# Kernel tuning notes

Hardware: AMD Instinct MI355X
Metric: run time of the kernel (lower is better)

Reference implementation:

```python
import math
import jax, jax.numpy as jnp
import numpy as np

D, NH, NL, NP = 256, 8, 3, 4
HD = D // NH
SHAPES = np.array([[92, 92], [46, 46], [23, 23]], dtype=np.int32)
LSI = np.concatenate([[0], np.cumsum(SHAPES[:, 0] * SHAPES[:, 1])[:-1]]).astype(np.int32)
LV = int((SHAPES[:, 0] * SHAPES[:, 1]).sum())  # 11109
B, LQ = 2, LV


def setup_inputs() -> dict:
    key = jax.random.key(0)
    ks = jax.random.split(key, 8)
    query = jax.random.normal(ks[0], (B, LQ, D), jnp.float32)
    reference_points = jax.random.uniform(ks[1], (B, LQ, NL, 2), dtype=jnp.float32)
    value_flat = jax.random.normal(ks[2], (B, LV, D), jnp.float32)
    # sampling_offsets: small random weight + structured directional bias (as in _reset_parameters)
    W_off = jax.random.normal(ks[3], (D, NH * NL * NP * 2), jnp.float32) * 0.01
    thetas = np.arange(NH, dtype=np.float64) * (2.0 * math.pi / NH)
    g = np.stack([np.cos(thetas), np.sin(thetas)], axis=-1)
    g = g / np.abs(g).max(axis=-1, keepdims=True)
    g = np.tile(g[:, None, None, :], (1, NL, NP, 1))
    g = g * (np.arange(NP) + 1)[None, None, :, None]
    b_off = jnp.asarray(g.reshape(-1), jnp.float32)
    W_attn = jax.random.normal(ks[4], (D, NH * NL * NP), jnp.float32) * 0.01
    b_attn = jnp.zeros((NH * NL * NP,), jnp.float32)
    W_val = jax.random.normal(ks[5], (D, D), jnp.float32) * (1.0 / math.sqrt(D))
    b_val = jnp.zeros((D,), jnp.float32)
    W_out = jax.random.normal(ks[6], (D, D), jnp.float32) * (1.0 / math.sqrt(D))
    b_out = jnp.zeros((D,), jnp.float32)
    return dict(query=query, reference_points=reference_points, value_flat=value_flat,
                W_val=W_val, b_val=b_val, W_off=W_off, b_off=b_off,
                W_attn=W_attn, b_attn=b_attn, W_out=W_out, b_out=b_out,
                spatial_shapes=jnp.asarray(SHAPES), level_start_index=jnp.asarray(LSI))


def _bilinear_sample(val_l, grid):
    """torch.F.grid_sample(mode='bilinear', padding_mode='zeros', align_corners=False).
    val_l: [B,H,W,nH,hd]; grid: [B,Q,nH,P,2] with (x,y) in [-1,1].
    Returns [B,nH,Q,P,hd]."""
    Bq, H, W, nH, hd = val_l.shape
    Q, P = grid.shape[1], grid.shape[3]
    x = ((grid[..., 0] + 1.0) * W - 1.0) * 0.5   # pixel coords, align_corners=False
    y = ((grid[..., 1] + 1.0) * H - 1.0) * 0.5
    x0f, y0f = jnp.floor(x), jnp.floor(y)
    lx, ly = x - x0f, y - y0f
    x0, y0 = x0f.astype(jnp.int32), y0f.astype(jnp.int32)
    val_bh = val_l.transpose(0, 3, 1, 2, 4).reshape(Bq * nH, H * W, hd)

    def corner(yi, xi, w):
        valid = (xi >= 0) & (xi < W) & (yi >= 0) & (yi < H)
        idx = jnp.clip(yi, 0, H - 1) * W + jnp.clip(xi, 0, W - 1)   # [B,Q,nH,P]
        idx_bh = idx.transpose(0, 2, 1, 3).reshape(Bq * nH, Q * P)
        g = jnp.take_along_axis(val_bh, idx_bh[:, :, None], axis=1)  # [B*nH, Q*P, hd]
        wm = (w * valid.astype(w.dtype)).transpose(0, 2, 1, 3).reshape(Bq * nH, Q * P, 1)
        return g * wm

    out = (corner(y0, x0, (1 - ly) * (1 - lx)) + corner(y0, x0 + 1, (1 - ly) * lx)
           + corner(y0 + 1, x0, ly * (1 - lx)) + corner(y0 + 1, x0 + 1, ly * lx))
    return out.reshape(Bq, nH, Q, P, hd)


def reference(query, reference_points, value_flat, W_val, b_val, W_off, b_off,
              W_attn, b_attn, W_out, b_out, spatial_shapes, level_start_index):
    shapes = np.asarray(spatial_shapes)          # static level geometry
    starts = np.asarray(level_start_index)
    Bq, Lq, _ = query.shape
    value = (value_flat @ W_val + b_val).reshape(Bq, -1, NH, HD)
    off = (query @ W_off + b_off).reshape(Bq, Lq, NH, NL, NP, 2)        # (dy,dx) pixels
    aw = jax.nn.softmax((query @ W_attn + b_attn).reshape(Bq, Lq, NH, NL * NP), axis=-1)
    aw = aw.reshape(Bq, Lq, NH, NL, NP)
    sh_f = jnp.asarray(shapes, jnp.float32)                              # [L,2] = (H,W)
    norm_off = off / sh_f[None, None, None, :, None, :]
    loc = reference_points[:, :, None, :, None, :] + norm_off           # [B,Lq,NH,NL,NP,2] (y,x)
    grid = 2.0 * loc[..., ::-1] - 1.0                                    # (x,y) in [-1,1]
    out = jnp.zeros((Bq, Lq, NH, HD), query.dtype)
    for l in range(NL):
        H, W = int(shapes[l, 0]), int(shapes[l, 1])
        s = int(starts[l])
        val_l = value[:, s:s + H * W].reshape(Bq, H, W, NH, HD)
        sampled = _bilinear_sample(val_l, grid[:, :, :, l])              # [B,NH,Lq,NP,HD]
        out = out + jnp.einsum('bhqpc,bqhp->bqhc', sampled, aw[:, :, :, l])
    return out.reshape(Bq, Lq, D) @ W_out + b_out
```

## Files before the change

kernel.cpp:

```cpp
#include <hip/hip_runtime.h>

#define LQn   11109
#define MTOT  22218

typedef __attribute__((ext_vector_type(8))) short short8;
typedef __attribute__((ext_vector_type(4))) float f32x4;

__device__ __forceinline__ unsigned short f2bf(float f) {
  union { float f; unsigned int u; } v; v.f = f;
  unsigned int r = v.u + 0x7fffu + ((v.u >> 16) & 1u);
  return (unsigned short)(r >> 16);
}

__device__ __forceinline__ int xcd_swz(int bid, int nwg) {
  const int xcd = bid & 7, pos = bid >> 3;
  const int q = nwg >> 3, r = nwg & 7;
  return (xcd < r ? xcd * (q + 1) : r * (q + 1) + (xcd - r) * q) + pos;
}

__global__ __launch_bounds__(256) void prep_weights(
    const float* __restrict__ Wval, const float* __restrict__ Woff,
    const float* __restrict__ Wattn, const float* __restrict__ Wout,
    const float* __restrict__ boff, const float* __restrict__ battn,
    unsigned short* __restrict__ Wval_t, unsigned short* __restrict__ Wcat_t,
    unsigned short* __restrict__ Wout_t, float* __restrict__ bcat) {
  int i = blockIdx.x * 256 + threadIdx.x;
  int n = i >> 8, k = i & 255;
  if (n < 256) {
    Wval_t[i] = f2bf(Wval[k * 256 + n]);
    Wout_t[i] = f2bf(Wout[k * 256 + n]);
  }
  float src = (n < 192) ? Woff[k * 192 + n] : Wattn[k * 96 + (n - 192)];
  Wcat_t[i] = f2bf(src);
  if (i < 288) bcat[i] = (i < 192) ? boff[i] : battn[i - 192];
}

__global__ __launch_bounds__(256) void gemm_fused12(
    const float* __restrict__ Aval,
    const float* __restrict__ Aq,
    const unsigned short* __restrict__ Bval,
    const unsigned short* __restrict__ Bcat,
    const float* __restrict__ bval, const float* __restrict__ bcat,
    unsigned short* __restrict__ value16,
    float* __restrict__ logits) {
  __shared__ unsigned short As[64][40];
  __shared__ unsigned short Bs[64][40];

  const int bm = blockIdx.x;
  int bn = blockIdx.y;
  const bool is2 = bn >= 4;
  if (is2) bn -= 4;
  const float* __restrict__ A = is2 ? Aq : Aval;
  const unsigned short* __restrict__ Bt = is2 ? Bcat : Bval;
  const float* __restrict__ bias = is2 ? bcat : bval;
  const int N = is2 ? 288 : 256;

  const int t = threadIdx.x;
  const int wave = t >> 6, lane = t & 63;
  const int wm = wave >> 1, wn = wave & 1;
  const int quad = lane >> 4, l16 = lane & 15;

  const int ldr = t >> 2;
  const int ldk = (t & 3) * 8;
  const int arow = bm * 64 + ldr;
  const int brow = bn * 64 + ldr;
  const bool aok = arow < MTOT;
  const bool bok = brow < N;
  const float* ap = A + (size_t)arow * 256 + ldk;
  const unsigned short* bp = Bt + (size_t)brow * 256 + ldk;

  f32x4 acc[2][2];
  for (int i = 0; i < 2; i++)
    for (int j = 0; j < 2; j++) acc[i][j] = (f32x4){0.f, 0.f, 0.f, 0.f};

  float4 a0c = {0.f,0.f,0.f,0.f}, a1c = a0c, a0n = a0c, a1n = a0c;
  uint4 bvc = {0u,0u,0u,0u}, bvn = bvc;
  if (aok) { a0c = *(const float4*)(ap);      a1c = *(const float4*)(ap + 4);
             a0n = *(const float4*)(ap + 32); a1n = *(const float4*)(ap + 36); }
  if (bok) { bvc = *(const uint4*)(bp);       bvn = *(const uint4*)(bp + 32); }

#pragma unroll
  for (int kb = 0; kb < 8; kb++) {
    ushort4 lo, hi;
    lo.x = f2bf(a0c.x); lo.y = f2bf(a0c.y); lo.z = f2bf(a0c.z); lo.w = f2bf(a0c.w);
    hi.x = f2bf(a1c.x); hi.y = f2bf(a1c.y); hi.z = f2bf(a1c.z); hi.w = f2bf(a1c.w);
    __syncthreads();
    *(ushort4*)(&As[ldr][ldk]) = lo;
    *(ushort4*)(&As[ldr][ldk + 4]) = hi;
    *(uint4*)(&Bs[ldr][ldk]) = bvc;
    __syncthreads();
    a0c = a0n; a1c = a1n; bvc = bvn;
    if (kb < 6) {
      const int k2 = (kb + 2) * 32;
      if (aok) { a0n = *(const float4*)(ap + k2); a1n = *(const float4*)(ap + k2 + 4); }
      if (bok) bvn = *(const uint4*)(bp + k2);
    }
    short8 af[2], bfr[2];
    for (int i = 0; i < 2; i++)
      af[i] = *(const short8*)(&As[wm * 32 + i * 16 + l16][quad * 8]);
    for (int j = 0; j < 2; j++)
      bfr[j] = *(const short8*)(&Bs[wn * 32 + j * 16 + l16][quad * 8]);
    for (int i = 0; i < 2; i++)
      for (int j = 0; j < 2; j++)
        acc[i][j] = __builtin_amdgcn_mfma_f32_16x16x32_bf16(af[i], bfr[j], acc[i][j], 0, 0, 0);
  }

  for (int i = 0; i < 2; i++)
    for (int j = 0; j < 2; j++) {
      int colg = bn * 64 + wn * 32 + j * 16 + l16;
      if (colg >= N) continue;
      float bsv = bias[colg];
      int row0 = bm * 64 + wm * 32 + i * 16 + quad * 4;
      for (int r = 0; r < 4; r++) {
        int rg = row0 + r;
        if (rg >= MTOT) continue;
        float v = acc[i][j][r] + bsv;
        if (is2) logits[(size_t)rg * 288 + colg] = v;
        else     value16[(size_t)rg * 256 + colg] = f2bf(v);
      }
    }
}

__global__ __launch_bounds__(256) void gemm_a16(
    const unsigned short* __restrict__ A,
    const unsigned short* __restrict__ Bt,
    const float* __restrict__ bias,
    float* __restrict__ C) {
  __shared__ unsigned short As[64][40];
  __shared__ unsigned short Bs[64][40];

  const int t = threadIdx.x;
  const int bm = blockIdx.x, bn = blockIdx.y;
  const int wave = t >> 6, lane = t & 63;
  const int wm = wave >> 1, wn = wave & 1;
  const int quad = lane >> 4, l16 = lane & 15;

  const int ldr = t >> 2;
  const int ldk = (t & 3) * 8;
  const int arow = bm * 64 + ldr;
  const int brow = bn * 64 + ldr;
  const bool aok = arow < MTOT;
  const unsigned short* ap = A + (size_t)arow * 256 + ldk;
  const unsigned short* bp = Bt + (size_t)brow * 256 + ldk;

  f32x4 acc[2][2];
  for (int i = 0; i < 2; i++)
    for (int j = 0; j < 2; j++) acc[i][j] = (f32x4){0.f, 0.f, 0.f, 0.f};

  uint4 avc = {0u,0u,0u,0u}, avn = avc, bvc, bvn;
  if (aok) { avc = *(const uint4*)(ap); avn = *(const uint4*)(ap + 32); }
  bvc = *(const uint4*)(bp);
  bvn = *(const uint4*)(bp + 32);

#pragma unroll
  for (int kb = 0; kb < 8; kb++) {
    __syncthreads();
    *(uint4*)(&As[ldr][ldk]) = avc;
    *(uint4*)(&Bs[ldr][ldk]) = bvc;
    __syncthreads();
    avc = avn; bvc = bvn;
    if (kb < 6) {
      const int k2 = (kb + 2) * 32;
      if (aok) avn = *(const uint4*)(ap + k2);
      bvn = *(const uint4*)(bp + k2);
    }
    short8 af[2], bfr[2];
    for (int i = 0; i < 2; i++)
      af[i] = *(const short8*)(&As[wm * 32 + i * 16 + l16][quad * 8]);
    for (int j = 0; j < 2; j++)
      bfr[j] = *(const short8*)(&Bs[wn * 32 + j * 16 + l16][quad * 8]);
    for (int i = 0; i < 2; i++)
      for (int j = 0; j < 2; j++)
        acc[i][j] = __builtin_amdgcn_mfma_f32_16x16x32_bf16(af[i], bfr[j], acc[i][j], 0, 0, 0);
  }

  for (int i = 0; i < 2; i++)
    for (int j = 0; j < 2; j++) {
      int colg = bn * 64 + wn * 32 + j * 16 + l16;
      float bsv = bias[colg];
      int row0 = bm * 64 + wm * 32 + i * 16 + quad * 4;
      for (int r = 0; r < 4; r++) {
        int rg = row0 + r;
        if (rg < MTOT)
          __builtin_nontemporal_store(acc[i][j][r] + bsv, &C[(size_t)rg * 256 + colg]);
      }
    }
}

__global__ __launch_bounds__(256) void msda_sample4(
    const unsigned short* __restrict__ value16,
    const float* __restrict__ logits,
    const float* __restrict__ refp,
    unsigned short* __restrict__ sampled) {
  __shared__ float          tw[8][96][4];
  __shared__ unsigned short ti[8][96][4];
  __shared__ float hmx[8][8], hrd[8][8];
  __shared__ float rfs[8][6];

  const int t = threadIdx.x;
  const int nbid = xcd_swz(blockIdx.x, gridDim.x);
  const int qbase = nbid * 8;

  if (t < 48) {
    int q = t / 6;
    if (qbase + q < MTOT) rfs[q][t - q * 6] = refp[(size_t)qbase * 6 + t];
  }
  if (t >= 64 && t < 128) {
    int tt = t - 64;
    int q = tt >> 3, h = tt & 7;
    int bq = qbase + q;
    if (bq < MTOT) {
      const float* lrow = logits + (size_t)bq * 288 + 192 + h * 12;
      float mx = -1e30f;
#pragma unroll
      for (int i = 0; i < 12; i++) mx = fmaxf(mx, __builtin_nontemporal_load(&lrow[i]));
      float den = 0.f;
#pragma unroll
      for (int i = 0; i < 12; i++)
        den += __expf(__builtin_nontemporal_load(&lrow[i]) - mx);
      hmx[q][h] = mx;
      hrd[q][h] = 1.0f / den;
    }
  }
  __syncthreads();

  {
    const int Hs[3] = {92, 46, 23};
    const int Ss[3] = {0, 8464, 10580};
#pragma unroll
    for (int r = 0; r < 3; r++) {
      const int task = t + r * 256;
      const int q = task / 96, s = task - q * 96;
      const int bq = qbase + q;
      if (bq < MTOT) {
        const int h = s / 12, pl = s - h * 12;
        const int l = pl >> 2;
        const int H = Hs[l], W = Hs[l], S = Ss[l];
        const float* lrow = logits + (size_t)bq * 288;
        const float aw = __expf(__builtin_nontemporal_load(&lrow[192 + s]) - hmx[q][h]) * hrd[q][h];
        const float offy = __builtin_nontemporal_load(&lrow[2 * s]);
        const float offx = __builtin_nontemporal_load(&lrow[2 * s + 1]);
        const float x = rfs[q][l * 2 + 1] * W + offx - 0.5f;
        const float y = rfs[q][l * 2 + 0] * H + offy - 0.5f;
        const float xf = floorf(x), yf = floorf(y);
        const int x0 = (int)xf, y0 = (int)yf;
        const float lx = x - xf, ly = y - yf;
        const bool xv0 = (x0 >= 0) & (x0 < W), xv1 = (x0 + 1 >= 0) & (x0 + 1 < W);
        const bool yv0 = (y0 >= 0) & (y0 < H), yv1 = (y0 + 1 >= 0) & (y0 + 1 < H);
        const int xc0 = min(max(x0, 0), W - 1), xc1 = min(max(x0 + 1, 0), W - 1);
        const int yc0 = min(max(y0, 0), H - 1), yc1 = min(max(y0 + 1, 0), H - 1);
        const int slot = pl * 8 + h;
        ti[q][slot][0] = (unsigned short)(S + yc0 * W + xc0);
        ti[q][slot][1] = (unsigned short)(S + yc0 * W + xc1);
        ti[q][slot][2] = (unsigned short)(S + yc1 * W + xc0);
        ti[q][slot][3] = (unsigned short)(S + yc1 * W + xc1);
        tw[q][slot][0] = (yv0 & xv0) ? aw * (1.f - ly) * (1.f - lx) : 0.f;
        tw[q][slot][1] = (yv0 & xv1) ? aw * (1.f - ly) * lx : 0.f;
        tw[q][slot][2] = (yv1 & xv0) ? aw * ly * (1.f - lx) : 0.f;
        tw[q][slot][3] = (yv1 & xv1) ? aw * ly * lx : 0.f;
      }
    }
  }
  __syncthreads();

  {
    const int w = t >> 6, lane = t & 63;
    const int q = w * 2 + (lane >> 5);
    const int h = (lane >> 2) & 7, cg = lane & 3;
    const int bq = qbase + q;
    const bool qv = bq < MTOT;
    const int bqc = qv ? bq : 0;
    const char* __restrict__ vb =
        (const char*)value16 + (size_t)(bqc / LQn) * ((size_t)LQn * 512);
    const unsigned laneoff = (unsigned)h * 64u + (unsigned)cg * 16u;

    float a0 = 0.f, a1 = 0.f, a2 = 0.f, a3 = 0.f;
    float a4 = 0.f, a5 = 0.f, a6 = 0.f, a7 = 0.f;
#pragma unroll
    for (int p = 0; p < 12; p++) {
      const int slot = p * 8 + h;
      const ushort4 tiv = *(const ushort4*)(&ti[q][slot][0]);
      const f32x4 wv = *(const f32x4*)(&tw[q][slot][0]);
#pragma unroll
      for (int k = 0; k < 4; k++) {
        const unsigned pix =
            (k == 0) ? tiv.x : (k == 1) ? tiv.y : (k == 2) ? tiv.z : tiv.w;
        const float wgt = wv[k];
        const uint4 u = *(const uint4*)(vb + ((pix << 9) + laneoff));
        a0 += wgt * __uint_as_float(u.x << 16);
        a1 += wgt * __uint_as_float(u.x & 0xffff0000u);
        a2 += wgt * __uint_as_float(u.y << 16);
        a3 += wgt * __uint_as_float(u.y & 0xffff0000u);
        a4 += wgt * __uint_as_float(u.z << 16);
        a5 += wgt * __uint_as_float(u.z & 0xffff0000u);
        a6 += wgt * __uint_as_float(u.w << 16);
        a7 += wgt * __uint_as_float(u.w & 0xffff0000u);
      }
    }
    if (qv) {
      uint4 o;
      o.x = (unsigned)f2bf(a0) | ((unsigned)f2bf(a1) << 16);
      o.y = (unsigned)f2bf(a2) | ((unsigned)f2bf(a3) << 16);
      o.z = (unsigned)f2bf(a4) | ((unsigned)f2bf(a5) << 16);
      o.w = (unsigned)f2bf(a6) | ((unsigned)f2bf(a7) << 16);
      *(uint4*)(sampled + (size_t)bq * 256 + h * 32 + cg * 8) = o;
    }
  }
}

extern "C" void kernel_launch(void* const* d_in, const int* in_sizes, int n_in,
                              void* d_out, int out_size, void* d_ws, size_t ws_size,
                              hipStream_t stream) {
  const float* query      = (const float*)d_in[0];
  const float* refp       = (const float*)d_in[1];
  const float* value_flat = (const float*)d_in[2];
  const float* W_val      = (const float*)d_in[3];
  const float* b_val      = (const float*)d_in[4];
  const float* W_off      = (const float*)d_in[5];
  const float* b_off      = (const float*)d_in[6];
  const float* W_attn     = (const float*)d_in[7];
  const float* b_attn     = (const float*)d_in[8];
  const float* W_out      = (const float*)d_in[9];
  const float* b_out      = (const float*)d_in[10];

  char* w = (char*)d_ws;
  size_t o = 0;
  auto carve = [&](size_t bytes) -> void* {
    void* p = (void*)(w + o);
    o += (bytes + 255) & ~(size_t)255;
    return p;
  };
  unsigned short* Wval_t  = (unsigned short*)carve(256 * 256 * 2);
  unsigned short* Wcat_t  = (unsigned short*)carve(288 * 256 * 2);
  unsigned short* Wout_t  = (unsigned short*)carve(256 * 256 * 2);
  float*          bcat    = (float*)carve(288 * 4);
  unsigned short* value16 = (unsigned short*)carve((size_t)MTOT * 256 * 2);
  float*          logits  = (float*)carve((size_t)MTOT * 288 * 4);
  unsigned short* samp_bf = (unsigned short*)carve((size_t)MTOT * 256 * 2);

  prep_weights<<<288, 256, 0, stream>>>(W_val, W_off, W_attn, W_out, b_off, b_attn,
                                        Wval_t, Wcat_t, Wout_t, bcat);

  const int mg = (MTOT + 63) / 64;
  dim3 g12(mg, 9);
  gemm_fused12<<<g12, 256, 0, stream>>>(value_flat, query, Wval_t, Wcat_t,
                                        b_val, bcat, value16, logits);

  const int sgrid = (MTOT + 7) / 8;
  msda_sample4<<<sgrid, 256, 0, stream>>>(value16, logits, refp, samp_bf);

  dim3 g3(mg, 4);
  gemm_a16<<<g3, 256, 0, stream>>>(samp_bf, Wout_t, b_out, (float*)d_out);
}
```

Before: 191.2 us.

## Fuse output projection GEMM into sampling kernel via shared-memory tile

The deformable-attention sampling kernel now writes its 8 query rows of bf16 samples into a shared-memory tile, reusing the weight/index scratch space. It then performs the output projection with MFMA directly from that tile, streaming W_out from global memory. This removes the intermediate sampled buffer round-trip and one kernel launch. The cost is that each block of 8 queries uses a 16-row MFMA with half the rows wasted and rereads the whole 256x256 W_out, relying on L2 hits. Nontemporal loads on logits are also replaced with ordinary loads.

```diff
diff --git a/kernel.cpp b/kernel.cpp
--- a/kernel.cpp
+++ b/kernel.cpp
@@ -121,79 +121,17 @@
     }
 }
 
-__global__ __launch_bounds__(256) void gemm_a16(
-    const unsigned short* __restrict__ A,
-    const unsigned short* __restrict__ Bt,
-    const float* __restrict__ bias,
-    float* __restrict__ C) {
-  __shared__ unsigned short As[64][40];
-  __shared__ unsigned short Bs[64][40];
-
-  const int t = threadIdx.x;
-  const int bm = blockIdx.x, bn = blockIdx.y;
-  const int wave = t >> 6, lane = t & 63;
-  const int wm = wave >> 1, wn = wave & 1;
-  const int quad = lane >> 4, l16 = lane & 15;
-
-  const int ldr = t >> 2;
-  const int ldk = (t & 3) * 8;
-  const int arow = bm * 64 + ldr;
-  const int brow = bn * 64 + ldr;
-  const bool aok = arow < MTOT;
-  const unsigned short* ap = A + (size_t)arow * 256 + ldk;
-  const unsigned short* bp = Bt + (size_t)brow * 256 + ldk;
-
-  f32x4 acc[2][2];
-  for (int i = 0; i < 2; i++)
-    for (int j = 0; j < 2; j++) acc[i][j] = (f32x4){0.f, 0.f, 0.f, 0.f};
-
-  uint4 avc = {0u,0u,0u,0u}, avn = avc, bvc, bvn;
-  if (aok) { avc = *(const uint4*)(ap); avn = *(const uint4*)(ap + 32); }
-  bvc = *(const uint4*)(bp);
-  bvn = *(const uint4*)(bp + 32);
-
-#pragma unroll
-  for (int kb = 0; kb < 8; kb++) {
-    __syncthreads();
-    *(uint4*)(&As[ldr][ldk]) = avc;
-    *(uint4*)(&Bs[ldr][ldk]) = bvc;
-    __syncthreads();
-    avc = avn; bvc = bvn;
-    if (kb < 6) {
-      const int k2 = (kb + 2) * 32;
-      if (aok) avn = *(const uint4*)(ap + k2);
-      bvn = *(const uint4*)(bp + k2);
-    }
-    short8 af[2], bfr[2];
-    for (int i = 0; i < 2; i++)
-      af[i] = *(const short8*)(&As[wm * 32 + i * 16 + l16][quad * 8]);
-    for (int j = 0; j < 2; j++)
-      bfr[j] = *(const short8*)(&Bs[wn * 32 + j * 16 + l16][quad * 8]);
-    for (int i = 0; i < 2; i++)
-      for (int j = 0; j < 2; j++)
-        acc[i][j] = __builtin_amdgcn_mfma_f32_16x16x32_bf16(af[i], bfr[j], acc[i][j], 0, 0, 0);
-  }
-
-  for (int i = 0; i < 2; i++)
-    for (int j = 0; j < 2; j++) {
-      int colg = bn * 64 + wn * 32 + j * 16 + l16;
-      float bsv = bias[colg];
-      int row0 = bm * 64 + wm * 32 + i * 16 + quad * 4;
-      for (int r = 0; r < 4; r++) {
-        int rg = row0 + r;
-        if (rg < MTOT)
-          __builtin_nontemporal_store(acc[i][j][r] + bsv, &C[(size_t)rg * 256 + colg]);
-      }
-    }
-}
-
-__global__ __launch_bounds__(256) void msda_sample4(
+__global__ __launch_bounds__(256) void msda_fused(
     const unsigned short* __restrict__ value16,
     const float* __restrict__ logits,
     const float* __restrict__ refp,
-    unsigned short* __restrict__ sampled) {
-  __shared__ float          tw[8][96][4];
-  __shared__ unsigned short ti[8][96][4];
+    const unsigned short* __restrict__ Wout,
+    const float* __restrict__ bout,
+    float* __restrict__ out) {
+  __shared__ char pool[18432];
+  float          (*tw)[96][4] = (float(*)[96][4])pool;
+  unsigned short (*ti)[96][4] = (unsigned short(*)[96][4])(pool + 12288);
+  unsigned short (*samp)[264] = (unsigned short(*)[264])pool;
   __shared__ float hmx[8][8], hrd[8][8];
   __shared__ float rfs[8][6];
 
@@ -213,11 +151,10 @@
       const float* lrow = logits + (size_t)bq * 288 + 192 + h * 12;
       float mx = -1e30f;
 #pragma unroll
-      for (int i = 0; i < 12; i++) mx = fmaxf(mx, __builtin_nontemporal_load(&lrow[i]));
+      for (int i = 0; i < 12; i++) mx = fmaxf(mx, lrow[i]);
       float den = 0.f;
 #pragma unroll
-      for (int i = 0; i < 12; i++)
-        den += __expf(__builtin_nontemporal_load(&lrow[i]) - mx);
+      for (int i = 0; i < 12; i++) den += __expf(lrow[i] - mx);
       hmx[q][h] = mx;
       hrd[q][h] = 1.0f / den;
     }
@@ -237,9 +174,8 @@
         const int l = pl >> 2;
         const int H = Hs[l], W = Hs[l], S = Ss[l];
         const float* lrow = logits + (size_t)bq * 288;
-        const float aw = __expf(__builtin_nontemporal_load(&lrow[192 + s]) - hmx[q][h]) * hrd[q][h];
-        const float offy = __builtin_nontemporal_load(&lrow[2 * s]);
-        const float offx = __builtin_nontemporal_load(&lrow[2 * s + 1]);
+        const float aw = __expf(lrow[192 + s] - hmx[q][h]) * hrd[q][h];
+        const float offy = lrow[2 * s], offx = lrow[2 * s + 1];
         const float x = rfs[q][l * 2 + 1] * W + offx - 0.5f;
         const float y = rfs[q][l * 2 + 0] * H + offy - 0.5f;
         const float xf = floorf(x), yf = floorf(y);
@@ -297,13 +233,41 @@
         a7 += wgt * __uint_as_float(u.w & 0xffff0000u);
       }
     }
-    if (qv) {
-      uint4 o;
-      o.x = (unsigned)f2bf(a0) | ((unsigned)f2bf(a1) << 16);
-      o.y = (unsigned)f2bf(a2) | ((unsigned)f2bf(a3) << 16);
-      o.z = (unsigned)f2bf(a4) | ((unsigned)f2bf(a5) << 16);
-      o.w = (unsigned)f2bf(a6) | ((unsigned)f2bf(a7) << 16);
-      *(uint4*)(sampled + (size_t)bq * 256 + h * 32 + cg * 8) = o;
+    uint4 o;
+    o.x = (unsigned)f2bf(a0) | ((unsigned)f2bf(a1) << 16);
+    o.y = (unsigned)f2bf(a2) | ((unsigned)f2bf(a3) << 16);
+    o.z = (unsigned)f2bf(a4) | ((unsigned)f2bf(a5) << 16);
+    o.w = (unsigned)f2bf(a6) | ((unsigned)f2bf(a7) << 16);
+
+    __syncthreads();
+    *(uint4*)(&samp[q][h * 32 + cg * 8]) = o;
+  }
+  __syncthreads();
+
+  {
+    const int w = t >> 6, lane = t & 63;
+    const int quad = lane >> 4, l16 = lane & 15;
+    const int n0 = w * 64;
+#pragma unroll
+    for (int j = 0; j < 4; j++) {
+      const int colg = n0 + j * 16 + l16;
+      const unsigned short* bp = Wout + (size_t)colg * 256 + quad * 8;
+      f32x4 acc = (f32x4){0.f, 0.f, 0.f, 0.f};
+#pragma unroll
+      for (int kb = 0; kb < 8; kb++) {
+        const short8 af = *(const short8*)(&samp[l16][kb * 32 + quad * 8]);
+        const short8 bf = *(const short8*)(bp + kb * 32);
+        acc = __builtin_amdgcn_mfma_f32_16x16x32_bf16(af, bf, acc, 0, 0, 0);
+      }
+      if (quad < 2) {
+        const float bsv = bout[colg];
+#pragma unroll
+        for (int r = 0; r < 4; r++) {
+          const int rg = qbase + quad * 4 + r;
+          if (rg < MTOT)
+            __builtin_nontemporal_store(acc[r] + bsv, &out[(size_t)rg * 256 + colg]);
+        }
+      }
     }
   }
 }
@@ -336,7 +300,6 @@
   float*          bcat    = (float*)carve(288 * 4);
   unsigned short* value16 = (unsigned short*)carve((size_t)MTOT * 256 * 2);
   float*          logits  = (float*)carve((size_t)MTOT * 288 * 4);
-  unsigned short* samp_bf = (unsigned short*)carve((size_t)MTOT * 256 * 2);
 
   prep_weights<<<288, 256, 0, stream>>>(W_val, W_off, W_attn, W_out, b_off, b_attn,
                                         Wval_t, Wcat_t, Wout_t, bcat);
@@ -347,8 +310,6 @@
                                         b_val, bcat, value16, logits);
 
   const int sgrid = (MTOT + 7) / 8;
-  msda_sample4<<<sgrid, 256, 0, stream>>>(value16, logits, refp, samp_bf);
-
-  dim3 g3(mg, 4);
-  gemm_a16<<<g3, 256, 0, stream>>>(samp_bf, Wout_t, b_out, (float*)d_out);
-}
+  msda_fused<<<sgrid, 256, 0, stream>>>(value16, logits, refp, Wout_t, b_out,
+                                        (float*)d_out);
+}
```

Result: slower. 211.5 us (+10.6%).
